# Optimization experiments

Measured on AMD Instinct MI355X. Metric: run time of the kernel, lower is better.

Reference implementation:

```python
import jax, jax.numpy as jnp
import numpy as np

DIM = 1024
H = 16
HD = DIM // H           # head_dim = 64
BS = 64                 # block_size
SPARSITY = 0.95
SCALE = HD ** -0.5


def setup_inputs() -> dict:
    key = jax.random.key(0)
    k1, k2, k3 = jax.random.split(key, 3)
    B, N = 2, 2048
    x = jax.random.normal(k1, (B, N, DIM), jnp.float32)
    # nn.Linear weights (out_features, in_features); qkv has no bias (qkv_bias=False)
    qkv_w = jax.random.normal(k2, (3 * DIM, DIM), jnp.float32) * (DIM ** -0.5)
    proj_w = jax.random.normal(k3, (DIM, DIM), jnp.float32) * (DIM ** -0.5)
    proj_b = jnp.zeros((DIM,), jnp.float32)
    return {"x": x, "qkv_w": qkv_w, "proj_w": proj_w, "proj_b": proj_b}


def reference(x, qkv_w, proj_w, proj_b):
    B, N, D = x.shape
    # qkv projection -> q,k,v each [B,H,N,HD]
    qkv = (x @ qkv_w.T).reshape(B, N, 3, H, HD).transpose(2, 0, 3, 1, 4)
    q, k, v = qkv[0], qkv[1], qkv[2]

    # --- CoarseCurvaturePredictor: block-level affinity + top-k block keep ---
    M = N // BS  # number of blocks (N divisible by block_size here)
    qb = q.reshape(B, H, M, BS, HD).mean(axis=3)  # [B,H,M,HD] coarse queries
    kb = k.reshape(B, H, M, BS, HD).mean(axis=3)  # [B,H,M,HD] coarse keys
    c = jnp.einsum('bhmd,bhnd->bhmn', qb, kb) * SCALE  # block scores [B,H,M,M]
    k_keep = max(1, int(round(M * (1.0 - SPARSITY))))  # blocks kept per row
    thresh = jax.lax.top_k(c, k_keep)[0][..., -1:]
    block_mask = (c >= thresh) | jnp.eye(M, dtype=bool)  # always keep diagonal

    # --- expand block mask to token level (repeat_interleave) ---
    tmask = jnp.repeat(jnp.repeat(block_mask, BS, axis=2), BS, axis=3)  # [B,H,N,N]

    # --- manual dense masked attention (faithful to fallback path) ---
    scores = jnp.einsum('bhqd,bhkd->bhqk', q, k) * SCALE
    scores = jnp.where(tmask, scores, -jnp.inf)
    probs = jax.nn.softmax(scores, axis=-1)
    out = jnp.einsum('bhqk,bhkd->bhqd', probs, v)
    out = out.transpose(0, 2, 1, 3).reshape(B, N, D)
    return out @ proj_w.T + proj_b
```

## Files before the change

### kernel.cpp

```cpp
#include <hip/hip_runtime.h>
#include <hip/hip_bf16.h>

#define BB 2
#define NN 2048
#define DIMD 1024
#define HH 16
#define HD64 64
#define MB 32
#define SCALE_F 0.125f

typedef __attribute__((ext_vector_type(8))) short bf16x8;
typedef __attribute__((ext_vector_type(8))) short short8v;
typedef __attribute__((ext_vector_type(4))) float f32x4;
typedef _Float16 f16;
typedef __attribute__((ext_vector_type(8))) _Float16 f16x8;

#define LSTR 72

#define VM_WAIT4 asm volatile("s_waitcnt vmcnt(4)" ::: "memory")
#define VM_WAIT3 asm volatile("s_waitcnt vmcnt(3)" ::: "memory")
#define VM_WAIT0 asm volatile("s_waitcnt vmcnt(0)" ::: "memory")
#define SBAR __builtin_amdgcn_s_barrier()
#define SCHED0 __builtin_amdgcn_sched_barrier(0)

__device__ __forceinline__ unsigned short bf16_hi(float f) {
    return __builtin_bit_cast(unsigned short, __float2bfloat16(f));
}
__device__ __forceinline__ float bf16_val(unsigned short u) {
    return __bfloat162float(__builtin_bit_cast(__hip_bfloat16, u));
}
__device__ __forceinline__ short f16_bits(float f) {
    return __builtin_bit_cast(short, (f16)f);
}
__device__ __forceinline__ void async_copy16(const void* g, void* l) {
    __builtin_amdgcn_global_load_lds((const __attribute__((address_space(1))) void*)g,
                                     (__attribute__((address_space(3))) void*)l, 16, 0, 0);
}


__global__ __launch_bounds__(256) void split_in_fused_kernel(
    const float* __restrict__ x, short* __restrict__ Axs,
    const float* __restrict__ w, short* __restrict__ Wqs,
    const float* __restrict__ pw, short* __restrict__ Wp)
{
    const int bid = blockIdx.x;
    const float* src; short* dst; int idx;
    if (bid < 4096)      { src = x;  dst = Axs; idx = bid * 256 + threadIdx.x; }
    else if (bid < 7168) { src = w;  dst = Wqs; idx = (bid - 4096) * 256 + threadIdx.x; }
    else                 { src = pw; dst = Wp;  idx = (bid - 7168) * 256 + threadIdx.x; }
    int e = idx * 4;
    float4 v = *(const float4*)(src + e);
    ushort4 o = make_ushort4((unsigned short)f16_bits(v.x), (unsigned short)f16_bits(v.y),
                             (unsigned short)f16_bits(v.z), (unsigned short)f16_bits(v.w));
    *(ushort4*)(dst + e) = o;
}

__global__ __launch_bounds__(256) void qkv_mfma_kernel(
    const short* __restrict__ A, const short* __restrict__ W,
    short* __restrict__ QhI, short* __restrict__ KhI, short* __restrict__ VtI,
    float* __restrict__ qbf, float* __restrict__ kbf)
{
    __shared__ short SM[16640];
    const int wg = blockIdx.x;
    const int row0 = (wg / 24) * 128;
    const int col0 = (wg % 24) * 128;
    const int tid = threadIdx.x;
    const int lane = tid & 63;
    const int wave = tid >> 6;
    const int wm = wave & 1, wn = wave >> 1;

    auto AHS = [&](int b) { return SM + b * 4096; };
    auto WHS = [&](int b) { return SM + 8192 + b * 4096; };

    f32x4 acc[4][4];
    const f32x4 zero = {0.f, 0.f, 0.f, 0.f};
    #pragma unroll
    for (int i = 0; i < 4; ++i)
        #pragma unroll
        for (int j = 0; j < 4; ++j) acc[i][j] = zero;

    const int ldr = lane >> 2;
    const int lko = (((lane & 3) ^ ((lane >> 3) & 3))) * 8;
    const int rsl = ((lane >> 4) ^ ((lane >> 1) & 3)) * 8;

    auto stage = [&](int bufi, int ktn) {
        const int kk = ktn << 5;
        #pragma unroll
        for (int i = 0; i < 2; ++i) {
            const int chunk = wave * 2 + i;
            const short* gA = A + (size_t)(row0 + chunk * 16 + ldr) * 1024 + kk + lko;
            const short* gW = W + (size_t)(col0 + chunk * 16 + ldr) * 1024 + kk + lko;
            async_copy16(gA, (char*)AHS(bufi) + chunk * 1024);
            async_copy16(gW, (char*)WHS(bufi) + chunk * 1024);
        }
    };

    auto compute = [&](int bufi) {
        const short* Ah = AHS(bufi);
        const short* Wh = WHS(bufi);
        f16x8 ah[4], wh[4];
        #pragma unroll
        for (int mi = 0; mi < 4; ++mi)
            ah[mi] = *(const f16x8*)(Ah + (wm * 64 + mi * 16 + (lane & 15)) * 32 + rsl);
        #pragma unroll
        for (int ni = 0; ni < 4; ++ni)
            wh[ni] = *(const f16x8*)(Wh + (wn * 64 + ni * 16 + (lane & 15)) * 32 + rsl);
        #pragma unroll
        for (int mi = 0; mi < 4; ++mi)
            #pragma unroll
            for (int ni = 0; ni < 4; ++ni)
                acc[mi][ni] = __builtin_amdgcn_mfma_f32_16x16x32_f16(ah[mi], wh[ni], acc[mi][ni], 0, 0, 0);
    };

    stage(0, 0);
    for (int kt = 0; kt < 30; kt += 2) {
        stage(1, kt + 1);
        VM_WAIT4; SBAR; SCHED0;
        compute(0);
        SBAR;
        stage(0, kt + 2);
        VM_WAIT4; SBAR; SCHED0;
        compute(1);
        SBAR;
    }
    stage(1, 31);
    VM_WAIT4; SBAR; SCHED0;
    compute(0);
    SBAR;
    VM_WAIT0; SBAR; SCHED0;
    compute(1);
    SBAR;

    const int gr_first = row0 + wm * 64;
    const int bb = gr_first >> 11;
    const int mblk = (gr_first & 2047) >> 6;
    const int gc0 = col0 + wn * 64;
    const int tsel = gc0 >> 10;
    const int h = (gc0 >> 6) & 15;
    const int tile = ((bb << 4) + h) * 32 + mblk;
    const float sc = (tsel == 0) ? SCALE_F : 1.0f;

    if (tsel != 2) {
        short* baseH = ((tsel == 0) ? QhI : KhI) + (size_t)tile * 4096;
        float* mdst  = ((tsel == 0) ? qbf : kbf) + ((size_t)((bb << 4) + h) * 32 + mblk) * 64;
        #pragma unroll
        for (int ni = 0; ni < 4; ++ni) {
            const int d = ni * 16 + (lane & 15);
            float colsum = 0.f;
            #pragma unroll
            for (int mi = 0; mi < 4; ++mi) {
                #pragma unroll
                for (int r = 0; r < 4; ++r) {
                    const int row = mi * 16 + (lane >> 4) * 4 + r;
                    float v = acc[mi][ni][r] * sc;
                    colsum += v;
                    const int off = (row * 64 + d) ^ ((row & 7) << 3);
                    baseH[off] = f16_bits(v);
                }
            }
            colsum += __shfl_xor(colsum, 16);
            colsum += __shfl_xor(colsum, 32);
            if ((lane >> 4) == 0) mdst[d] = colsum * (1.f / 64.f);
        }
    } else {
        short* tb = SM + wave * 4160;
        #pragma unroll
        for (int ni = 0; ni < 4; ++ni)
            #pragma unroll
            for (int mi = 0; mi < 4; ++mi)
                #pragma unroll
                for (int r = 0; r < 4; ++r) {
                    const int row = mi * 16 + (lane >> 4) * 4 + r;
                    const int d = ni * 16 + (lane & 15);
                    tb[row * 65 + d] = f16_bits(acc[mi][ni][r]);
                }
        short* vout = VtI + (size_t)tile * 4096;
        #pragma unroll
        for (int c = 0; c < 8; ++c) {
            short8v tv;
            #pragma unroll
            for (int j = 0; j < 8; ++j)
                tv[j] = tb[(c * 8 + j) * 65 + lane];
            const int off = (lane * 64 + c * 8) ^ ((lane & 7) << 3);
            *(short8v*)(vout + off) = tv;
        }
    }
}

__global__ __launch_bounds__(256) void scores_splitw_kernel(
    const float* __restrict__ qbf, const float* __restrict__ kbf,
    unsigned int* __restrict__ maskbits, float scale,
    const float* __restrict__ projw, short* __restrict__ Wdst)
{
    __shared__ float qs_[32][64];
    __shared__ float ks_[32][64];
    __shared__ float cb[32][32];
    const int bid = blockIdx.x;
    const int tid = threadIdx.x;

    if (bid >= 32) {
        int idx = (bid - 32) * 256 + tid;
        int e = idx * 4;
        float4 v = *(const float4*)(projw + e);
        ushort4 o = make_ushort4((unsigned short)f16_bits(v.x), (unsigned short)f16_bits(v.y),
                                 (unsigned short)f16_bits(v.z), (unsigned short)f16_bits(v.w));
        *(ushort4*)(Wdst + e) = o;
        return;
    }

    #pragma unroll
    for (int i = 0; i < 8; ++i) {
        int e = tid + i * 256;
        qs_[e >> 6][e & 63] = qbf[(size_t)bid * 2048 + e];
        ks_[e >> 6][e & 63] = kbf[(size_t)bid * 2048 + e];
    }
    __syncthreads();

    #pragma unroll
    for (int i = 0; i < 4; ++i) {
        int idx = tid + i * 256;
        int r = idx >> 5, c = idx & 31;
        float s = 0.f;
        #pragma unroll
        for (int d = 0; d < 64; ++d) s += qs_[r][d] * ks_[c][d];
        cb[r][c] = s * scale;
    }
    __syncthreads();

    if (tid < 32) {
        float m1 = -INFINITY, m2 = -INFINITY;
        for (int n = 0; n < 32; ++n) {
            float v = cb[tid][n];
            if (v > m1) { m2 = m1; m1 = v; }
            else if (v > m2) { m2 = v; }
        }
        unsigned int bits = 1u << tid;
        for (int n = 0; n < 32; ++n)
            if (cb[tid][n] >= m2) bits |= 1u << n;
        maskbits[bid * 32 + tid] = bits;
    }
}

__global__ __launch_bounds__(256) void proj_mfma_kernel(
    const short* __restrict__ A, const short* __restrict__ W,
    const float* __restrict__ bias, float* __restrict__ out)
{
    __shared__ short Ahs[2][128 * 32];
    __shared__ short Whs[2][64 * 32];
    const int bid = blockIdx.x;
    const int wg = (bid & 7) * 64 + (bid >> 3);
    const int row0 = (wg >> 4) * 128;
    const int col0 = (wg & 15) * 64;
    const int tid = threadIdx.x;
    const int lane = tid & 63;
    const int wave = tid >> 6;

    f32x4 acc[2][4];
    const f32x4 zero = {0.f, 0.f, 0.f, 0.f};
    #pragma unroll
    for (int i = 0; i < 2; ++i)
        #pragma unroll
        for (int j = 0; j < 4; ++j) acc[i][j] = zero;

    const int ldr = lane >> 2;
    const int lko = (((lane & 3) ^ ((lane >> 3) & 3))) * 8;
    const int rsl = ((lane >> 4) ^ ((lane >> 1) & 3)) * 8;

    auto stage = [&](int bufi, int ktn) {
        const int kk = ktn << 5;
        #pragma unroll
        for (int i = 0; i < 2; ++i) {
            const int chunk = wave * 2 + i;
            const short* gA = A + (size_t)(row0 + chunk * 16 + ldr) * 1024 + kk + lko;
            async_copy16(gA, (char*)&Ahs[bufi][0] + chunk * 1024);
        }
        {
            const short* gW = W + (size_t)(col0 + wave * 16 + ldr) * 1024 + kk + lko;
            async_copy16(gW, (char*)&Whs[bufi][0] + wave * 1024);
        }
    };

    auto compute = [&](int bufi) {
        const short* Ah = Ahs[bufi];
        const short* Wh = Whs[bufi];
        f16x8 ah[2], wh[4];
        #pragma unroll
        for (int mi = 0; mi < 2; ++mi)
            ah[mi] = *(const f16x8*)(Ah + (wave * 32 + mi * 16 + (lane & 15)) * 32 + rsl);
        #pragma unroll
        for (int ni = 0; ni < 4; ++ni)
            wh[ni] = *(const f16x8*)(Wh + (ni * 16 + (lane & 15)) * 32 + rsl);
        #pragma unroll
        for (int mi = 0; mi < 2; ++mi)
            #pragma unroll
            for (int ni = 0; ni < 4; ++ni)
                acc[mi][ni] = __builtin_amdgcn_mfma_f32_16x16x32_f16(ah[mi], wh[ni], acc[mi][ni], 0, 0, 0);
    };

    stage(0, 0);
    for (int kt = 0; kt < 30; kt += 2) {
        stage(1, kt + 1);
        VM_WAIT3; SBAR; SCHED0;
        compute(0);
        SBAR;
        stage(0, kt + 2);
        VM_WAIT3; SBAR; SCHED0;
        compute(1);
        SBAR;
    }
    stage(1, 31);
    VM_WAIT3; SBAR; SCHED0;
    compute(0);
    SBAR;
    VM_WAIT0; SBAR; SCHED0;
    compute(1);

    #pragma unroll
    for (int ni = 0; ni < 4; ++ni) {
        int gc = col0 + ni * 16 + (lane & 15);
        float bv = bias[gc];
        #pragma unroll
        for (int mi = 0; mi < 2; ++mi) {
            int gr0 = row0 + wave * 32 + mi * 16 + (lane >> 4) * 4;
            #pragma unroll
            for (int r = 0; r < 4; ++r)
                out[(size_t)(gr0 + r) * 1024 + gc] = acc[mi][ni][r] + bv;
        }
    }
}

__global__ __launch_bounds__(256) void sparse_attn_mfma_kernel(
    const short* __restrict__ QhI, const short* __restrict__ KhI,
    const short* __restrict__ VtI, const unsigned int* __restrict__ maskbits,
    short* __restrict__ aout)
{
    __shared__ f16 Qh[4096];
    __shared__ f16 Kh[2][4096];
    __shared__ f16 Vt[2][4096];
    __shared__ f16 Pb[64 * LSTR];

    const int bid = blockIdx.x;
    const int wg = (bid & 7) * 128 + (bid >> 3);
    const int m  = wg & 31;
    const int bh = wg >> 5;
    const int b  = bh >> 4, h = bh & 15;
    const int tid = threadIdx.x;
    const int lane = tid & 63;
    const int wave = tid >> 6;
    const f32x4 zero = {0.f, 0.f, 0.f, 0.f};

    const unsigned int mask = maskbits[bh * 32 + m];

    {
        const size_t qt = (size_t)(bh * 32 + m) * 4096;
        const int so = wave * 1024 + lane * 8;
        async_copy16(QhI + qt + so,       (char*)Qh + wave * 2048);
        async_copy16(QhI + qt + so + 512, (char*)Qh + wave * 2048 + 1024);
    }

    auto stageKV = [&](int bufi, int nb) {
        const size_t t4 = (size_t)(bh * 32 + nb) * 4096;
        const int so = wave * 1024 + lane * 8;
        async_copy16(KhI + t4 + so,       (char*)&Kh[bufi][0] + wave * 2048);
        async_copy16(KhI + t4 + so + 512, (char*)&Kh[bufi][0] + wave * 2048 + 1024);
        async_copy16(VtI + t4 + so,       (char*)&Vt[bufi][0] + wave * 2048);
        async_copy16(VtI + t4 + so + 512, (char*)&Vt[bufi][0] + wave * 2048 + 1024);
    };

    f32x4 o_acc[4];
    float macc[4], lacc[4];
    #pragma unroll
    for (int r = 0; r < 4; ++r) { macc[r] = -INFINITY; lacc[r] = 0.f; }
    #pragma unroll
    for (int t = 0; t < 4; ++t) o_acc[t] = zero;

    const int arow = wave * 16 + (lane & 15);
    const int kofs = (lane >> 4) * 8;
    const int colb = (lane >> 4) * 16;

    auto computeTile = [&](int bi) {
        const f16* KhB = &Kh[bi][0];
        f32x4 s_acc[4];
        #pragma unroll
        for (int t = 0; t < 4; ++t) s_acc[t] = zero;
        #pragma unroll
        for (int c = 0; c < 2; ++c) {
            const int qoff = (arow * 128 + c * 64 + colb) ^ ((arow & 7) << 4);
            f16x8 ah = *(const f16x8*)((const char*)Qh + qoff);
            #pragma unroll
            for (int t = 0; t < 4; ++t) {
                const int krow = t * 16 + (lane & 15);
                const int koff = (krow * 128 + c * 64 + colb) ^ ((krow & 7) << 4);
                f16x8 bh_ = *(const f16x8*)((const char*)KhB + koff);
                s_acc[t] = __builtin_amdgcn_mfma_f32_16x16x32_f16(ah, bh_, s_acc[t], 0, 0, 0);
            }
        }

        float alpha[4], psum[4];
        #pragma unroll
        for (int r = 0; r < 4; ++r) {
            float v0 = fmaxf(fmaxf(s_acc[0][r], s_acc[1][r]), fmaxf(s_acc[2][r], s_acc[3][r]));
            #pragma unroll
            for (int off = 1; off < 16; off <<= 1)
                v0 = fmaxf(v0, __shfl_xor(v0, off));
            float mnew = fmaxf(macc[r], v0);
            alpha[r] = expf(macc[r] - mnew);
            macc[r] = mnew;
            psum[r] = 0.f;
        }
        #pragma unroll
        for (int t = 0; t < 4; ++t) {
            #pragma unroll
            for (int r = 0; r < 4; ++r) {
                float p = expf(s_acc[t][r] - macc[r]);
                psum[r] += p;
                Pb[(wave * 16 + (lane >> 4) * 4 + r) * LSTR + t * 16 + (lane & 15)] = (f16)p;
            }
        }
        #pragma unroll
        for (int r = 0; r < 4; ++r) {
            float v0 = psum[r];
            #pragma unroll
            for (int off = 1; off < 16; off <<= 1) v0 += __shfl_xor(v0, off);
            lacc[r] = lacc[r] * alpha[r] + v0;
            #pragma unroll
            for (int t = 0; t < 4; ++t) o_acc[t][r] *= alpha[r];
        }

        const f16* VtB = &Vt[bi][0];
        #pragma unroll
        for (int c = 0; c < 2; ++c) {
            f16x8 af = *(const f16x8*)(Pb + arow * LSTR + c * 32 + kofs);
            #pragma unroll
            for (int t = 0; t < 4; ++t) {
                const int vrow = t * 16 + (lane & 15);
                const int voff = (vrow * 128 + c * 64 + colb) ^ ((vrow & 7) << 4);
                f16x8 bf = *(const f16x8*)((const char*)VtB + voff);
                o_acc[t] = __builtin_amdgcn_mfma_f32_16x16x32_f16(af, bf, o_acc[t], 0, 0, 0);
            }
        }
    };

    unsigned int mm = mask;
    int nb0 = __builtin_ctz(mm); mm &= mm - 1;
    stageKV(0, nb0);
    int cur = 0;
    for (;;) {
        int nb_nxt = -1;
        if (mm) { nb_nxt = __builtin_ctz(mm); mm &= mm - 1; stageKV(cur ^ 1, nb_nxt); }
        if (nb_nxt >= 0) { VM_WAIT4; } else { VM_WAIT0; }
        SBAR; SCHED0;
        computeTile(cur);
        SBAR;
        if (nb_nxt < 0) break;
        cur ^= 1;
    }

    float inv[4];
    #pragma unroll
    for (int r = 0; r < 4; ++r) inv[r] = (lacc[r] > 0.f) ? (1.f / lacc[r]) : 0.f;
    #pragma unroll
    for (int t = 0; t < 4; ++t) {
        int gc = h * 64 + t * 16 + (lane & 15);
        #pragma unroll
        for (int r = 0; r < 4; ++r) {
            int grow = b * NN + m * 64 + wave * 16 + (lane >> 4) * 4 + r;
            float v = o_acc[t][r] * inv[r];
            aout[(size_t)grow * 1024 + gc] = f16_bits(v);
        }
    }
}


__global__ __launch_bounds__(256) void block_mean_kernel(
    const float* __restrict__ qf, const float* __restrict__ kf,
    float* __restrict__ qbf, float* __restrict__ kbf)
{
    int idx = blockIdx.x * 256 + threadIdx.x;
    const float* src = (idx < 65536) ? qf : kf;
    float* dst       = (idx < 65536) ? qbf : kbf;
    int e = idx & 65535;
    int d = e & 63;
    int r = e >> 6;
    size_t base = (size_t)r * 4096 + d;
    float s = 0.f;
    #pragma unroll
    for (int i = 0; i < 64; ++i) s += src[base + (size_t)i * 64];
    dst[e] = s * (1.f / 64.f);
}

__global__ __launch_bounds__(256) void qkv_gemm_fb(
    const float* __restrict__ x, const float* __restrict__ w,
    float* __restrict__ qf, float* __restrict__ kf, float* __restrict__ vf)
{
    __shared__ float As[64][33];
    __shared__ float Bs[64][33];
    const int tid = threadIdx.x;
    const int row0 = blockIdx.y * 64;
    const int col0 = blockIdx.x * 64;
    const int ty = tid >> 4, tx = tid & 15;

    float acc[4][4] = {};
    for (int k0 = 0; k0 < 1024; k0 += 32) {
        #pragma unroll
        for (int i = 0; i < 8; ++i) {
            int e = tid + i * 256;
            int r = e >> 5, c = e & 31;
            As[r][c] = x[(size_t)(row0 + r) * 1024 + k0 + c];
            Bs[r][c] = w[(size_t)(col0 + r) * 1024 + k0 + c];
        }
        __syncthreads();
        #pragma unroll
        for (int kk = 0; kk < 32; ++kk) {
            float a[4], bq[4];
            #pragma unroll
            for (int i = 0; i < 4; ++i) a[i] = As[ty * 4 + i][kk];
            #pragma unroll
            for (int j = 0; j < 4; ++j) bq[j] = Bs[tx * 4 + j][kk];
            #pragma unroll
            for (int i = 0; i < 4; ++i)
                #pragma unroll
                for (int j = 0; j < 4; ++j)
                    acc[i][j] += a[i] * bq[j];
        }
        __syncthreads();
    }

    const int tsel = col0 >> 10;
    const int h    = (col0 & 1023) >> 6;
    float* dstbuf = (tsel == 0) ? qf : (tsel == 1) ? kf : vf;
    #pragma unroll
    for (int i = 0; i < 4; ++i) {
        int row = row0 + ty * 4 + i;
        int b   = row >> 11, n = row & 2047;
        size_t rb = ((size_t)(b * HH + h) * NN + n) * HD64;
        #pragma unroll
        for (int j = 0; j < 4; ++j)
            dstbuf[rb + tx * 4 + j] = acc[i][j];
    }
}

__global__ __launch_bounds__(256) void proj_gemm_fb(
    const float* __restrict__ attn, const float* __restrict__ w,
    const float* __restrict__ bias, float* __restrict__ out)
{
    __shared__ float As[64][33];
    __shared__ float Bs[64][33];
    const int tid = threadIdx.x;
    const int row0 = blockIdx.y * 64;
    const int col0 = blockIdx.x * 64;
    const int ty = tid >> 4, tx = tid & 15;

    float acc[4][4] = {};
    for (int k0 = 0; k0 < 1024; k0 += 32) {
        #pragma unroll
        for (int i = 0; i < 8; ++i) {
            int e = tid + i * 256;
            int r = e >> 5, c = e & 31;
            As[r][c] = attn[(size_t)(row0 + r) * 1024 + k0 + c];
            Bs[r][c] = w[(size_t)(col0 + r) * 1024 + k0 + c];
        }
        __syncthreads();
        #pragma unroll
        for (int kk = 0; kk < 32; ++kk) {
            float a[4], bq[4];
            #pragma unroll
            for (int i = 0; i < 4; ++i) a[i] = As[ty * 4 + i][kk];
            #pragma unroll
            for (int j = 0; j < 4; ++j) bq[j] = Bs[tx * 4 + j][kk];
            #pragma unroll
            for (int i = 0; i < 4; ++i)
                #pragma unroll
                for (int j = 0; j < 4; ++j)
                    acc[i][j] += a[i] * bq[j];
        }
        __syncthreads();
    }

    #pragma unroll
    for (int j = 0; j < 4; ++j) {
        int col = col0 + tx * 4 + j;
        float bv = bias[col];
        #pragma unroll
        for (int i = 0; i < 4; ++i) {
            int row = row0 + ty * 4 + i;
            out[(size_t)row * 1024 + col] = acc[i][j] + bv;
        }
    }
}

__global__ __launch_bounds__(256) void sparse_attn_fb(
    const float* __restrict__ qf, const float* __restrict__ kf,
    const float* __restrict__ vf, const unsigned int* __restrict__ maskbits,
    float* __restrict__ attnf)
{
    __shared__ float kbuf[64][64];
    __shared__ float vbuf[64][64];
    __shared__ float sbuf[64][65];
    const int m  = blockIdx.x & 31;
    const int bh = blockIdx.x >> 5;
    const int b  = bh >> 4, h = bh & 15;
    const int t  = threadIdx.x;
    const int qr = t >> 2;
    const int dg = t & 3;
    const int d0 = dg * 16;

    float qreg[16];
    {
        const float* qp = qf + ((size_t)bh * NN + m * 64 + qr) * HD64 + d0;
        #pragma unroll
        for (int j = 0; j < 16; j += 4) {
            float4 v = *(const float4*)(qp + j);
            qreg[j] = v.x; qreg[j+1] = v.y; qreg[j+2] = v.z; qreg[j+3] = v.w;
        }
    }

    const unsigned int mask = maskbits[bh * 32 + m];
    float macc = -INFINITY, lacc = 0.f;
    float oacc[16];
    #pragma unroll
    for (int j = 0; j < 16; ++j) oacc[j] = 0.f;

    for (int nb = 0; nb < 32; ++nb) {
        if (!((mask >> nb) & 1u)) continue;
        __syncthreads();
        {
            const float* gk = kf + ((size_t)bh * NN + nb * 64) * HD64;
            const float* gv = vf + ((size_t)bh * NN + nb * 64) * HD64;
            #pragma unroll
            for (int i = 0; i < 4; ++i) {
                async_copy16(gk + t * 4 + i * 1024, (char*)kbuf + t * 16 + i * 4096);
                async_copy16(gv + t * 4 + i * 1024, (char*)vbuf + t * 16 + i * 4096);
            }
        }
        __syncthreads();

        float bmax = -INFINITY;
        for (int kk = 0; kk < 64; ++kk) {
            float s = 0.f;
            #pragma unroll
            for (int j = 0; j < 16; ++j) s += qreg[j] * kbuf[kk][d0 + j];
            s += __shfl_xor(s, 1);
            s += __shfl_xor(s, 2);
            s *= SCALE_F;
            if (dg == 0) sbuf[qr][kk] = s;
            bmax = fmaxf(bmax, s);
        }
        float mnew  = fmaxf(macc, bmax);
        float alpha = expf(macc - mnew);
        lacc *= alpha;
        #pragma unroll
        for (int j = 0; j < 16; ++j) oacc[j] *= alpha;
        for (int kk = 0; kk < 64; ++kk) {
            float p = expf(sbuf[qr][kk] - mnew);
            lacc += p;
            #pragma unroll
            for (int j = 0; j < 16; ++j) oacc[j] += p * vbuf[kk][d0 + j];
        }
        macc = mnew;
    }

    float inv = (lacc > 0.f) ? (1.f / lacc) : 0.f;
    size_t orow = ((size_t)(b * NN + m * 64 + qr)) * DIMD + h * 64 + d0;
    #pragma unroll
    for (int j = 0; j < 16; ++j) attnf[orow + j] = oacc[j] * inv;
}

extern "C" void kernel_launch(void* const* d_in, const int* in_sizes, int n_in,
                              void* d_out, int out_size, void* d_ws, size_t ws_size,
                              hipStream_t stream)
{
    const float* x      = (const float*)d_in[0];
    const float* qkv_w  = (const float*)d_in[1];
    const float* proj_w = (const float*)d_in[2];
    const float* proj_b = (const float*)d_in[3];
    float* out = (float*)d_out;

    short* QhI = (short*)d_ws;
    short* KhI = QhI + 4194304;
    short* VtI = KhI + 4194304;
    float* qbf = (float*)(VtI + 4194304);
    float* kbf = qbf + 65536;
    unsigned int* maskb = (unsigned int*)(kbf + 65536);
    short* Axs = (short*)(maskb + 1024);
    short* Wqs = Axs + (size_t)4096 * 1024;
    short* Wp  = Wqs + (size_t)3072 * 1024;
    const size_t need_fast = (size_t)((char*)(Wp + (size_t)1024 * 1024) - (char*)d_ws);

    if (ws_size >= need_fast) {
        split_in_fused_kernel<<<8192, 256, 0, stream>>>(x, Axs, qkv_w, Wqs, proj_w, Wp);
        qkv_mfma_kernel<<<768, 256, 0, stream>>>(Axs, Wqs, QhI, KhI, VtI, qbf, kbf);
        scores_splitw_kernel<<<32, 256, 0, stream>>>(qbf, kbf, maskb, 1.0f,
                                                     (const float*)nullptr, (short*)nullptr);
        sparse_attn_mfma_kernel<<<1024, 256, 0, stream>>>(QhI, KhI, VtI, maskb, Axs);
        proj_mfma_kernel<<<512, 256, 0, stream>>>(Axs, Wp, proj_b, out);
    } else {
        float* qf2  = (float*)d_ws;
        float* kf2  = qf2 + 4194304;
        float* vf2  = kf2 + 4194304;
        float* qbf2 = vf2 + 4194304;
        float* kbf2 = qbf2 + 65536;
        unsigned int* maskb2 = (unsigned int*)(kbf2 + 65536);
        float* attnf = (float*)(maskb2 + 1024);
        qkv_gemm_fb<<<dim3(48, 64), 256, 0, stream>>>(x, qkv_w, qf2, kf2, vf2);
        block_mean_kernel<<<512, 256, 0, stream>>>(qf2, kf2, qbf2, kbf2);
        scores_splitw_kernel<<<32, 256, 0, stream>>>(qbf2, kbf2, maskb2, SCALE_F,
                                                     (const float*)nullptr, (short*)nullptr);
        sparse_attn_fb<<<1024, 256, 0, stream>>>(qf2, kf2, vf2, maskb2, attnf);
        proj_gemm_fb<<<dim3(16, 64), 256, 0, stream>>>(attnf, proj_w, proj_b, out);
    }
}
```

Before: 183.9 us.

## Fuse block-score top-k mask computation into sparse attention kernel

Drops the separate scores kernel launch. Each attention workgroup now computes its own row of coarse block scores with a lane-per-key-block dot product, then finds the top-2 threshold with wave shuffles and ballots. The diagonal K/V tile is prefetched before the mask is computed, so the load overlaps the score computation. In exchange, the score work is repeated by all four waves of each workgroup, and the top-2 selection assumes k_keep equals 2, which is hard-coded.

Result: faster. 160.6 us (-12.7%).

```diff
diff --git a/kernel.cpp b/kernel.cpp
--- a/kernel.cpp
+++ b/kernel.cpp
@@ -331,7 +331,8 @@
 
 __global__ __launch_bounds__(256) void sparse_attn_mfma_kernel(
     const short* __restrict__ QhI, const short* __restrict__ KhI,
-    const short* __restrict__ VtI, const unsigned int* __restrict__ maskbits,
+    const short* __restrict__ VtI,
+    const float* __restrict__ qbf, const float* __restrict__ kbf,
     short* __restrict__ aout)
 {
     __shared__ f16 Qh[4096];
@@ -349,8 +350,6 @@
     const int wave = tid >> 6;
     const f32x4 zero = {0.f, 0.f, 0.f, 0.f};
 
-    const unsigned int mask = maskbits[bh * 32 + m];
-
     {
         const size_t qt = (size_t)(bh * 32 + m) * 4096;
         const int so = wave * 1024 + lane * 8;
@@ -367,6 +366,30 @@
         async_copy16(VtI + t4 + so + 512, (char*)&Vt[bufi][0] + wave * 2048 + 1024);
     };
 
+    stageKV(0, m);
+
+    unsigned int mask;
+    {
+        float c = -INFINITY;
+        if (lane < 32) {
+            const float* qrow = qbf + ((size_t)bh * 32 + m) * 64;
+            const float* krow = kbf + ((size_t)bh * 32 + lane) * 64;
+            float s = 0.f;
+            for (int d = 0; d < 64; ++d) s += qrow[d] * krow[d];
+            c = s;
+        }
+        float m1 = c;
+        #pragma unroll
+        for (int off = 1; off < 64; off <<= 1) m1 = fmaxf(m1, __shfl_xor(m1, off));
+        unsigned long long eq = __ballot(c == m1);
+        float cx = (c == m1) ? -INFINITY : c;
+        #pragma unroll
+        for (int off = 1; off < 64; off <<= 1) cx = fmaxf(cx, __shfl_xor(cx, off));
+        float m2 = (__popcll(eq) >= 2) ? m1 : cx;
+        unsigned long long ge = __ballot(c >= m2);
+        mask = (unsigned int)(ge & 0xffffffffULL) | (1u << m);
+    }
+
     f32x4 o_acc[4];
     float macc[4], lacc[4];
     #pragma unroll
@@ -441,9 +464,7 @@
         }
     };
 
-    unsigned int mm = mask;
-    int nb0 = __builtin_ctz(mm); mm &= mm - 1;
-    stageKV(0, nb0);
+    unsigned int mm = mask & ~(1u << m);
     int cur = 0;
     for (;;) {
         int nb_nxt = -1;
@@ -690,9 +711,7 @@
     if (ws_size >= need_fast) {
         split_in_fused_kernel<<<8192, 256, 0, stream>>>(x, Axs, qkv_w, Wqs, proj_w, Wp);
         qkv_mfma_kernel<<<768, 256, 0, stream>>>(Axs, Wqs, QhI, KhI, VtI, qbf, kbf);
-        scores_splitw_kernel<<<32, 256, 0, stream>>>(qbf, kbf, maskb, 1.0f,
-                                                     (const float*)nullptr, (short*)nullptr);
-        sparse_attn_mfma_kernel<<<1024, 256, 0, stream>>>(QhI, KhI, VtI, maskb, Axs);
+        sparse_attn_mfma_kernel<<<1024, 256, 0, stream>>>(QhI, KhI, VtI, qbf, kbf, Axs);
         proj_mfma_kernel<<<512, 256, 0, stream>>>(Axs, Wp, proj_b, out);
     } else {
         float* qf2  = (float*)d_ws;
```
